# Optimization experiments

Hardware: AMD Instinct MI355X
Metric: run time of the kernel (lower is better)

Reference implementation:

```python
import jax, jax.numpy as jnp
import numpy as np

N = 20000      # num nodes
E = 320000     # num edges (before self loops)
DIN = 128      # in_channels
DH = 128       # hidden channels
C = 40         # num classes


def setup_inputs() -> dict:
    key = jax.random.key(0)
    ks = jax.random.split(key, 16)
    s_in = 1.0 / np.sqrt(DIN)
    s_h = 1.0 / np.sqrt(DH)
    s_a = 1.0 / np.sqrt(2 * DH)
    return {
        "x": jax.random.normal(ks[0], (N, DIN), jnp.float32),
        "edge_index": jax.random.randint(ks[1], (2, E), 0, N),
        "norm": jax.random.uniform(ks[2], (E + N,), jnp.float32),  # Jaccard sims in [0,1]
        # layer 1 params
        "W1": jax.random.uniform(ks[3], (DIN, DH), jnp.float32, -s_in, s_in),
        "aW1": jax.random.uniform(ks[4], (2 * DH, 1), jnp.float32, -s_a, s_a),
        "ab1": jax.random.uniform(ks[5], (1,), jnp.float32, -s_a, s_a),
        "alpha1": jnp.array([0.5], jnp.float32),
        "b1": jnp.zeros((DH,), jnp.float32),
        # layer 2 params
        "W2": jax.random.uniform(ks[6], (DH, DH), jnp.float32, -s_h, s_h),
        "aW2": jax.random.uniform(ks[7], (2 * DH, 1), jnp.float32, -s_a, s_a),
        "ab2": jax.random.uniform(ks[8], (1,), jnp.float32, -s_a, s_a),
        "alpha2": jnp.array([0.5], jnp.float32),
        "b2": jnp.zeros((DH,), jnp.float32),
        # output head
        "Wout": jax.random.uniform(ks[9], (DH, C), jnp.float32, -s_h, s_h),
        "bout": jax.random.uniform(ks[10], (C,), jnp.float32, -s_h, s_h),
    }


def _gat_layer(x, src, dst, norm, W, aW, ab, alpha, bias):
    n = x.shape[0]
    h = x @ W                              # [N, DH]
    s = h[src]                             # gathered source feats [E', DH]
    t = h[dst]                             # gathered target feats [E', DH]
    # attention logit per edge -> exp(leaky_relu(.))
    e = jnp.exp(jax.nn.leaky_relu(jnp.concatenate([s, t], axis=-1) @ aW + ab,
                                  negative_slope=0.2))          # [E', 1]
    e_sum = jax.ops.segment_sum(e, dst, num_segments=n)         # softmax denom per dst node
    a = e / e_sum[dst]
    s_sim = jnp.exp(norm)[:, None]                               # [E', 1]
    s_sum = jax.ops.segment_sum(s_sim, src, num_segments=n)     # note: summed over SRC (as in original)
    sw = s_sim / s_sum[dst]                                      # but indexed by DST (as in original)
    al = jnp.clip(alpha, 1e-4, 0.9999)
    w = al * a + (1.0 - al) * sw                                 # blended edge weight [E', 1]
    out = jax.ops.segment_max(w * s, dst, num_segments=n)        # aggr='max' propagate
    return out + bias


def reference(x, edge_index, norm, W1, aW1, ab1, alpha1, b1,
              W2, aW2, ab2, alpha2, b2, Wout, bout):
    n = x.shape[0]
    loops = jnp.arange(n, dtype=edge_index.dtype)
    src = jnp.concatenate([edge_index[0], loops])   # add_self_loops
    dst = jnp.concatenate([edge_index[1], loops])
    h = jax.nn.relu(_gat_layer(x, src, dst, norm, W1, aW1, ab1, alpha1, b1))
    h = jax.nn.relu(_gat_layer(h, src, dst, norm, W2, aW2, ab2, alpha2, b2))
    return jax.nn.log_softmax(h @ Wout + bout, axis=-1)
```

## Files before the change

kernel.cpp:

```cpp
#include <hip/hip_runtime.h>
#include <math.h>

#define DHID 128
#define NCLS 40
#define ELLW 64

typedef unsigned int   u32;
typedef unsigned short u16;

__device__ __forceinline__ u16 f2bf(float f) {
  u32 u = __float_as_uint(f);
  return (u16)((u + 0x7FFFu + ((u >> 16) & 1u)) >> 16);
}
__device__ __forceinline__ float bf_lo(u32 p) { return __uint_as_float(p << 16); }
__device__ __forceinline__ float bf_hi(u32 p) { return __uint_as_float(p & 0xFFFF0000u); }

__global__ __launch_bounds__(256) void zero_kernel(
    int* __restrict__ counts, float* __restrict__ ssum,
    int* __restrict__ ovf_cnt, int n) {
  int i = blockIdx.x * 256 + threadIdx.x;
  if (i < n) { counts[i] = 0; ssum[i] = 0.f; }
  if (i == 0) *ovf_cnt = 0;
}

__device__ __forceinline__ void gemm_from_lds(
    float* Ws, float* Xs, const float* __restrict__ W,
    const float* __restrict__ aW, u16* __restrict__ Hout,
    float* __restrict__ elo, float* __restrict__ ero, int n, int rowBase) {
  int t = threadIdx.x;
  int rg = t >> 5;
  int c0 = (t & 31) << 2;
  float acc[4][4];
#pragma unroll
  for (int j = 0; j < 4; ++j)
#pragma unroll
    for (int c = 0; c < 4; ++c) acc[j][c] = 0.f;

  for (int kt = 0; kt < 2; ++kt) {
    __syncthreads();
    const float* Wsrc = W + kt * 64 * DHID;
#pragma unroll
    for (int q = 0; q < 8; ++q) {
      int i4 = t + q * 256;
      *reinterpret_cast<float4*>(Ws + i4 * 4) =
          *reinterpret_cast<const float4*>(Wsrc + i4 * 4);
    }
    __syncthreads();
#pragma unroll 2
    for (int k = 0; k < 64; k += 4) {
      float4 xv[4];
#pragma unroll
      for (int j = 0; j < 4; ++j)
        xv[j] = *reinterpret_cast<const float4*>(
            Xs + (rg * 4 + j) * DHID + kt * 64 + k);
#pragma unroll
      for (int kk = 0; kk < 4; ++kk) {
        float4 wv = *reinterpret_cast<const float4*>(Ws + (k + kk) * DHID + c0);
#pragma unroll
        for (int j = 0; j < 4; ++j) {
          float xj = (&xv[j].x)[kk];
          acc[j][0] = fmaf(xj, wv.x, acc[j][0]);
          acc[j][1] = fmaf(xj, wv.y, acc[j][1]);
          acc[j][2] = fmaf(xj, wv.z, acc[j][2]);
          acc[j][3] = fmaf(xj, wv.w, acc[j][3]);
        }
      }
    }
  }

#pragma unroll
  for (int j = 0; j < 4; ++j) {
    int gr = rowBase + rg * 4 + j;
    if (gr < n) {
      ushort4 hv;
      hv.x = f2bf(acc[j][0]); hv.y = f2bf(acc[j][1]);
      hv.z = f2bf(acc[j][2]); hv.w = f2bf(acc[j][3]);
      *reinterpret_cast<ushort4*>(Hout + (size_t)gr * DHID + c0) = hv;
    }
  }

  float4 al4 = *reinterpret_cast<const float4*>(aW + c0);
  float4 ar4 = *reinterpret_cast<const float4*>(aW + DHID + c0);
  __syncthreads();
  float* P = Xs;
#pragma unroll
  for (int j = 0; j < 4; ++j) {
    int r = rg * 4 + j;
    float pl = acc[j][0] * al4.x + acc[j][1] * al4.y +
               acc[j][2] * al4.z + acc[j][3] * al4.w;
    float pr = acc[j][0] * ar4.x + acc[j][1] * ar4.y +
               acc[j][2] * ar4.z + acc[j][3] * ar4.w;
    P[r * 33 + (t & 31)] = pl;
    P[1056 + r * 33 + (t & 31)] = pr;
  }
  __syncthreads();
  if (t < 64) {
    int half = t >> 5, r = t & 31;
    const float* Pr = P + half * 1056 + r * 33;
    float s = 0.f;
#pragma unroll
    for (int c = 0; c < 32; ++c) s += Pr[c];
    int gr = rowBase + r;
    if (gr < n) { if (half) ero[gr] = s; else elo[gr] = s; }
  }
}

__device__ __forceinline__ void gemm_stage_x(
    float* Xs, const float* __restrict__ X, int n, int rowBase) {
  int t = threadIdx.x;
#pragma unroll
  for (int q = 0; q < 4; ++q) {
    int i4 = t + q * 256;
    int r = i4 >> 5, c = (i4 & 31) << 2;
    int gr = rowBase + r;
    float4 v = (gr < n)
        ? *reinterpret_cast<const float4*>(X + (size_t)gr * DHID + c)
        : make_float4(0.f, 0.f, 0.f, 0.f);
    *reinterpret_cast<float4*>(Xs + r * DHID + c) = v;
  }
}

__global__ __launch_bounds__(256) void gemm1_build_kernel(
    const float* __restrict__ X, const float* __restrict__ W,
    const float* __restrict__ aW, u16* __restrict__ H,
    float* __restrict__ el, float* __restrict__ er, int n, int gT,
    const int* __restrict__ ei, const float* __restrict__ norm,
    int* __restrict__ counts, float* __restrict__ ssum,
    uint2* __restrict__ ell, uint4* __restrict__ ovf,
    int* __restrict__ ovf_cnt, int E, int EP) {
  __shared__ float Ws[64 * 128];
  __shared__ float Xs[32 * 128];
  if (blockIdx.x < gT) {
    int rowBase = blockIdx.x * 32;
    gemm_stage_x(Xs, X, n, rowBase);
    gemm_from_lds(Ws, Xs, W, aW, H, el, er, n, rowBase);
  } else {
    int k = (blockIdx.x - gT) * 256 + threadIdx.x;
    if (k < EP) {
      int src, dst;
      if (k < E) { src = ei[k]; dst = ei[E + k]; }
      else       { src = dst = k - E; }
      float se = __expf(norm[k]);
      atomicAdd(&ssum[src], se);
      int slot = atomicAdd(&counts[dst], 1);
      if (slot < ELLW) {
        ell[(size_t)dst * ELLW + slot] =
            make_uint2((u32)src, __float_as_uint(se));
      } else {
        int o = atomicAdd(ovf_cnt, 1);
        ovf[o] = make_uint4((u32)dst, (u32)src, __float_as_uint(se), 0u);
      }
    }
  }
}

__global__ __launch_bounds__(256) void gemm_elr_kernel(
    const float* __restrict__ X, const float* __restrict__ W,
    const float* __restrict__ aW, u16* __restrict__ H,
    float* __restrict__ el, float* __restrict__ er, int n) {
  __shared__ float Ws[64 * 128];
  __shared__ float Xs[32 * 128];
  int rowBase = blockIdx.x * 32;
  gemm_stage_x(Xs, X, n, rowBase);
  gemm_from_lds(Ws, Xs, W, aW, H, el, er, n, rowBase);
}

__device__ __forceinline__ void agg_node8(
    const u16* __restrict__ H, const int* __restrict__ counts,
    const uint2* __restrict__ ell, const uint4* __restrict__ ovf, int ovfN,
    const float* __restrict__ el, const float* __restrict__ ssum,
    float base, float al, int node, int lane, float a[8]) {
  int deg = counts[node];
  int dell = deg < ELLW ? deg : ELLW;
  const uint2* erow = ell + (size_t)node * ELLW;
  int src0 = 0; float sx0 = 0.f;
  if (lane < dell) {
    uint2 rec = erow[lane];
    src0 = (int)rec.x;
    sx0  = __uint_as_float(rec.y);
  }
  int qw = lane >> 4;
  const u16* Hf = H + ((lane & 15) << 3);
  int ei0 = qw, ei1 = 4 + qw;
  int ci0 = ei0 < dell ? ei0 : 0;
  int ci1 = ei1 < dell ? ei1 : 0;
  int ps0 = __shfl(src0, ci0);
  int ps1 = __shfl(src0, ci1);
  uint4 pr0 = *reinterpret_cast<const uint4*>(Hf + (size_t)ps0 * DHID);
  uint4 pr1 = *reinterpret_cast<const uint4*>(Hf + (size_t)ps1 * DHID);
  float e0 = 0.f;
  if (lane < dell) {
    float g = el[src0] + base;
    e0 = __expf(g > 0.f ? g : 0.2f * g);
  }
  float es = e0;
  if (ovfN > 0 && deg > ELLW) {
    for (int cb = 0; cb < ovfN; cb += 64) {
      int i = cb + lane;
      if (i < ovfN) {
        uint4 r = ovf[i];
        if ((int)r.x == node) {
          float g = el[(int)r.y] + base;
          es += __expf(g > 0.f ? g : 0.2f * g);
        }
      }
    }
  }
#pragma unroll
  for (int off = 32; off; off >>= 1) es += __shfl_xor(es, off);
  float invEs = al / es;
  float omaS  = (1.f - al) / ssum[node];
  float w0 = e0 * invEs + sx0 * omaS;
#pragma unroll
  for (int i = 0; i < 8; ++i) a[i] = -INFINITY;
  {
    float wA = __shfl(w0, ci0);
    float wB = __shfl(w0, ci1);
    if (ei0 < dell) {
      a[0] = fmaxf(a[0], wA * bf_lo(pr0.x)); a[1] = fmaxf(a[1], wA * bf_hi(pr0.x));
      a[2] = fmaxf(a[2], wA * bf_lo(pr0.y)); a[3] = fmaxf(a[3], wA * bf_hi(pr0.y));
      a[4] = fmaxf(a[4], wA * bf_lo(pr0.z)); a[5] = fmaxf(a[5], wA * bf_hi(pr0.z));
      a[6] = fmaxf(a[6], wA * bf_lo(pr0.w)); a[7] = fmaxf(a[7], wA * bf_hi(pr0.w));
    }
    if (ei1 < dell) {
      a[0] = fmaxf(a[0], wB * bf_lo(pr1.x)); a[1] = fmaxf(a[1], wB * bf_hi(pr1.x));
      a[2] = fmaxf(a[2], wB * bf_lo(pr1.y)); a[3] = fmaxf(a[3], wB * bf_hi(pr1.y));
      a[4] = fmaxf(a[4], wB * bf_lo(pr1.z)); a[5] = fmaxf(a[5], wB * bf_hi(pr1.z));
      a[6] = fmaxf(a[6], wB * bf_lo(pr1.w)); a[7] = fmaxf(a[7], wB * bf_hi(pr1.w));
    }
  }
  int j = 8;
  for (; j + 7 < dell; j += 8) {
    int ea = j + qw, eb = j + 4 + qw;
    int   sa = __shfl(src0, ea); float wa = __shfl(w0, ea);
    int   sb = __shfl(src0, eb); float wb = __shfl(w0, eb);
    uint4 ha = *reinterpret_cast<const uint4*>(Hf + (size_t)sa * DHID);
    uint4 hb = *reinterpret_cast<const uint4*>(Hf + (size_t)sb * DHID);
    a[0] = fmaxf(a[0], fmaxf(wa * bf_lo(ha.x), wb * bf_lo(hb.x)));
    a[1] = fmaxf(a[1], fmaxf(wa * bf_hi(ha.x), wb * bf_hi(hb.x)));
    a[2] = fmaxf(a[2], fmaxf(wa * bf_lo(ha.y), wb * bf_lo(hb.y)));
    a[3] = fmaxf(a[3], fmaxf(wa * bf_hi(ha.y), wb * bf_hi(hb.y)));
    a[4] = fmaxf(a[4], fmaxf(wa * bf_lo(ha.z), wb * bf_lo(hb.z)));
    a[5] = fmaxf(a[5], fmaxf(wa * bf_hi(ha.z), wb * bf_hi(hb.z)));
    a[6] = fmaxf(a[6], fmaxf(wa * bf_lo(ha.w), wb * bf_lo(hb.w)));
    a[7] = fmaxf(a[7], fmaxf(wa * bf_hi(ha.w), wb * bf_hi(hb.w)));
  }
  for (; j < dell; j += 4) {
    int e = j + qw;
    int ec = e < dell ? e : dell - 1;
    int   sa = __shfl(src0, ec); float wa = __shfl(w0, ec);
    if (e < dell) {
      uint4 ha = *reinterpret_cast<const uint4*>(Hf + (size_t)sa * DHID);
      a[0] = fmaxf(a[0], wa * bf_lo(ha.x));
      a[1] = fmaxf(a[1], wa * bf_hi(ha.x));
      a[2] = fmaxf(a[2], wa * bf_lo(ha.y));
      a[3] = fmaxf(a[3], wa * bf_hi(ha.y));
      a[4] = fmaxf(a[4], wa * bf_lo(ha.z));
      a[5] = fmaxf(a[5], wa * bf_hi(ha.z));
      a[6] = fmaxf(a[6], wa * bf_lo(ha.w));
      a[7] = fmaxf(a[7], wa * bf_hi(ha.w));
    }
  }
  if (ovfN > 0 && deg > ELLW) {
    for (int cb = 0; cb < ovfN; cb += 64) {
      int i = cb + lane;
      uint4 r = (i < ovfN) ? ovf[i] : make_uint4(0u, 0u, 0u, 0u);
      bool match = (i < ovfN) && ((int)r.x == node);
      int si = (int)r.y;
      float wi = 0.f;
      if (match) {
        float g = el[si] + base;
        wi = __expf(g > 0.f ? g : 0.2f * g) * invEs +
             __uint_as_float(r.z) * omaS;
      }
      unsigned long long mask = __ballot(match);
      while (mask) {
        int jb = __ffsll(mask) - 1;
        mask &= mask - 1;
        int   sj = __shfl(si, jb);
        float wj = __shfl(wi, jb);
        uint4 h = *reinterpret_cast<const uint4*>(Hf + (size_t)sj * DHID);
        a[0] = fmaxf(a[0], wj * bf_lo(h.x)); a[1] = fmaxf(a[1], wj * bf_hi(h.x));
        a[2] = fmaxf(a[2], wj * bf_lo(h.y)); a[3] = fmaxf(a[3], wj * bf_hi(h.y));
        a[4] = fmaxf(a[4], wj * bf_lo(h.z)); a[5] = fmaxf(a[5], wj * bf_hi(h.z));
        a[6] = fmaxf(a[6], wj * bf_lo(h.w)); a[7] = fmaxf(a[7], wj * bf_hi(h.w));
      }
    }
  }
#pragma unroll
  for (int i = 0; i < 8; ++i) {
    a[i] = fmaxf(a[i], __shfl_xor(a[i], 16));
    a[i] = fmaxf(a[i], __shfl_xor(a[i], 32));
  }
}

__global__ __launch_bounds__(256) void agg_kernel(
    const u16* __restrict__ H, const int* __restrict__ counts,
    const uint2* __restrict__ ell, const uint4* __restrict__ ovf,
    const int* __restrict__ ovf_cnt, const float* __restrict__ el,
    const float* __restrict__ er, const float* __restrict__ ssum,
    const float* __restrict__ ab, const float* __restrict__ alpha,
    const float* __restrict__ bias, float* __restrict__ Y, int n) {
  int node = blockIdx.x * 4 + (threadIdx.x >> 6);
  int lane = threadIdx.x & 63;
  if (node >= n) return;
  int ovfN = *ovf_cnt;
  float al = fminf(fmaxf(alpha[0], 1e-4f), 0.9999f);
  float base = er[node] + ab[0];
  float a[8];
  agg_node8(H, counts, ell, ovf, ovfN, el, ssum, base, al, node, lane, a);
  if (lane < 16) {
    int fl = lane << 3;
    float4 b0 = *reinterpret_cast<const float4*>(bias + fl);
    float4 b1 = *reinterpret_cast<const float4*>(bias + fl + 4);
    float4 o0, o1;
    o0.x = fmaxf(a[0] + b0.x, 0.f); o0.y = fmaxf(a[1] + b0.y, 0.f);
    o0.z = fmaxf(a[2] + b0.z, 0.f); o0.w = fmaxf(a[3] + b0.w, 0.f);
    o1.x = fmaxf(a[4] + b1.x, 0.f); o1.y = fmaxf(a[5] + b1.y, 0.f);
    o1.z = fmaxf(a[6] + b1.z, 0.f); o1.w = fmaxf(a[7] + b1.w, 0.f);
    *reinterpret_cast<float4*>(Y + (size_t)node * DHID + fl) = o0;
    *reinterpret_cast<float4*>(Y + (size_t)node * DHID + fl + 4) = o1;
  }
}

__global__ __launch_bounds__(256) void agg_head_kernel(
    const u16* __restrict__ H, const int* __restrict__ counts,
    const uint2* __restrict__ ell, const uint4* __restrict__ ovf,
    const int* __restrict__ ovf_cnt, const float* __restrict__ el,
    const float* __restrict__ er, const float* __restrict__ ssum,
    const float* __restrict__ ab, const float* __restrict__ alpha,
    const float* __restrict__ bias, const float* __restrict__ Wout,
    const float* __restrict__ bout, float* __restrict__ out, int n) {
  __shared__ float Wl[DHID * NCLS];
  __shared__ float hl[4][DHID];
  int t = threadIdx.x;
  for (int i = t; i < DHID * NCLS; i += 256) Wl[i] = Wout[i];
  int wv = t >> 6, lane = t & 63;
  int node = blockIdx.x * 4 + wv;
  if (node < n) {
    int ovfN = *ovf_cnt;
    float al = fminf(fmaxf(alpha[0], 1e-4f), 0.9999f);
    float base = er[node] + ab[0];
    float a[8];
    agg_node8(H, counts, ell, ovf, ovfN, el, ssum, base, al, node, lane, a);
    if (lane < 16) {
      int fl = lane << 3;
#pragma unroll
      for (int i = 0; i < 8; ++i)
        hl[wv][fl + i] = fmaxf(a[i] + bias[fl + i], 0.f);
    }
  }
  __syncthreads();
  if (node >= n) return;
  float z = -INFINITY;
  bool act = lane < NCLS;
  if (act) {
    z = bout[lane];
    const float* hr = hl[wv];
#pragma unroll 8
    for (int k = 0; k < DHID; ++k) z = fmaf(hr[k], Wl[k * NCLS + lane], z);
  }
  float m = z;
#pragma unroll
  for (int off = 32; off; off >>= 1) m = fmaxf(m, __shfl_xor(m, off));
  float p = act ? expf(z - m) : 0.f;
#pragma unroll
  for (int off = 32; off; off >>= 1) p += __shfl_xor(p, off);
  float ls = logf(p);
  if (act) out[(size_t)node * NCLS + lane] = z - m - ls;
}

extern "C" void kernel_launch(void* const* d_in, const int* in_sizes, int n_in,
                              void* d_out, int out_size, void* d_ws, size_t ws_size,
                              hipStream_t stream) {
  const float* x     = (const float*)d_in[0];
  const int*   ei    = (const int*)d_in[1];
  const float* norm  = (const float*)d_in[2];
  const float* W1    = (const float*)d_in[3];
  const float* aW1   = (const float*)d_in[4];
  const float* ab1   = (const float*)d_in[5];
  const float* alpha1= (const float*)d_in[6];
  const float* b1    = (const float*)d_in[7];
  const float* W2    = (const float*)d_in[8];
  const float* aW2   = (const float*)d_in[9];
  const float* ab2   = (const float*)d_in[10];
  const float* alpha2= (const float*)d_in[11];
  const float* b2    = (const float*)d_in[12];
  const float* Wout  = (const float*)d_in[13];
  const float* bout  = (const float*)d_in[14];
  float* out = (float*)d_out;

  const int N  = in_sizes[0] / DHID;
  const int E  = in_sizes[1] / 2;
  const int EP = E + N;

  char* ws = (char*)d_ws;
  size_t off = 0;
  auto alloc = [&](size_t bytes) -> void* {
    void* p = ws + off;
    off += (bytes + 255) & ~(size_t)255;
    return p;
  };
  int*   counts  = (int*)  alloc((size_t)N * 4);
  float* ssum    = (float*)alloc((size_t)N * 4);
  int*   ovf_cnt = (int*)  alloc(256);
  u16*   Hbf     = (u16*)  alloc((size_t)N * DHID * 2);
  float* B       = (float*)alloc((size_t)N * DHID * 4);
  float* el      = (float*)alloc((size_t)N * 4);
  float* er      = (float*)alloc((size_t)N * 4);
  uint2* ell     = (uint2*)alloc((size_t)N * ELLW * 8);
  uint4* ovf     = (uint4*)alloc((size_t)EP * 16);

  const int gZero = (N + 255) / 256;
  const int gEdge = (EP + 255) / 256;
  const int gT    = (N + 31) / 32;
  const int gAgg  = (N + 3) / 4;

  zero_kernel<<<gZero, 256, 0, stream>>>(counts, ssum, ovf_cnt, N);
  gemm1_build_kernel<<<gT + gEdge, 256, 0, stream>>>(
      x, W1, aW1, Hbf, el, er, N, gT, ei, norm, counts, ssum, ell, ovf,
      ovf_cnt, E, EP);
  agg_kernel<<<gAgg, 256, 0, stream>>>(Hbf, counts, ell, ovf, ovf_cnt, el, er,
                                       ssum, ab1, alpha1, b1, B, N);
  gemm_elr_kernel<<<gT, 256, 0, stream>>>(B, W2, aW2, Hbf, el, er, N);
  agg_head_kernel<<<gAgg, 256, 0, stream>>>(Hbf, counts, ell, ovf, ovf_cnt,
                                            el, er, ssum, ab2, alpha2, b2,
                                            Wout, bout, out, N);
}
```

Before: 110.6 us.

## Use bf16 MFMA for node GEMMs with prepacked weights and bf16 activations

Replaces the fp32 LDS-tiled FMA GEMM with bf16 MFMA 16x16x32 instructions. A prep kernel now converts x to bf16, packs W1/W2 into MFMA fragment layout, and zeroes the counters. Layer-1 aggregation writes bf16 output so layer 2 reads half the bytes. This adds a conversion pass over x and lowers precision of the GEMM inputs, and leaves some dead code in the epilogue.

Result: faster. 104.7 us (-5.3%).

```diff
diff --git a/kernel.cpp b/kernel.cpp
--- a/kernel.cpp
+++ b/kernel.cpp
@@ -7,6 +7,8 @@
 
 typedef unsigned int   u32;
 typedef unsigned short u16;
+using short8 = __attribute__((ext_vector_type(8))) short;
+using f32x4  = __attribute__((ext_vector_type(4))) float;
 
 __device__ __forceinline__ u16 f2bf(float f) {
   u32 u = __float_as_uint(f);
@@ -15,125 +17,135 @@
 __device__ __forceinline__ float bf_lo(u32 p) { return __uint_as_float(p << 16); }
 __device__ __forceinline__ float bf_hi(u32 p) { return __uint_as_float(p & 0xFFFF0000u); }
 
-__global__ __launch_bounds__(256) void zero_kernel(
+__global__ __launch_bounds__(256) void prep_kernel(
+    const float* __restrict__ x, const float* __restrict__ W1,
+    const float* __restrict__ W2, u16* __restrict__ xbf,
+    u16* __restrict__ Wp1, u16* __restrict__ Wp2,
     int* __restrict__ counts, float* __restrict__ ssum,
-    int* __restrict__ ovf_cnt, int n) {
-  int i = blockIdx.x * 256 + threadIdx.x;
-  if (i < n) { counts[i] = 0; ssum[i] = 0.f; }
-  if (i == 0) *ovf_cnt = 0;
-}
-
-__device__ __forceinline__ void gemm_from_lds(
-    float* Ws, float* Xs, const float* __restrict__ W,
-    const float* __restrict__ aW, u16* __restrict__ Hout,
-    float* __restrict__ elo, float* __restrict__ ero, int n, int rowBase) {
+    int* __restrict__ ovf_cnt, int N) {
+  int gi = blockIdx.x * 256 + threadIdx.x;
+  int Ncvt = N * 16;
+  if (gi < Ncvt) {
+    int base = gi * 8;
+    float4 v0 = *reinterpret_cast<const float4*>(x + base);
+    float4 v1 = *reinterpret_cast<const float4*>(x + base + 4);
+    uint4 o;
+    o.x = (u32)f2bf(v0.x) | ((u32)f2bf(v0.y) << 16);
+    o.y = (u32)f2bf(v0.z) | ((u32)f2bf(v0.w) << 16);
+    o.z = (u32)f2bf(v1.x) | ((u32)f2bf(v1.y) << 16);
+    o.w = (u32)f2bf(v1.z) | ((u32)f2bf(v1.w) << 16);
+    *reinterpret_cast<uint4*>(xbf + base) = o;
+    return;
+  }
+  gi -= Ncvt;
+  if (gi < N) { counts[gi] = 0; ssum[gi] = 0.f; return; }
+  gi -= N;
+  if (gi < 32768) {
+    int layer = gi >> 14, q = gi & 16383;
+    int j = q & 7, l = (q >> 3) & 63, kt = (q >> 9) & 3, ct = q >> 11;
+    int k = kt * 32 + (l >> 4) * 8 + j;
+    int col = ct * 16 + (l & 15);
+    const float* Wsrc = layer ? W2 : W1;
+    u16* Wdst = layer ? Wp2 : Wp1;
+    Wdst[q] = f2bf(Wsrc[k * DHID + col]);
+    return;
+  }
+  gi -= 32768;
+  if (gi == 0) *ovf_cnt = 0;
+}
+
+__device__ __forceinline__ void mfma_gemm_block(
+    float* Cl, float* P, const u16* __restrict__ Xbf,
+    const u16* __restrict__ Wp, const float* __restrict__ aW,
+    u16* __restrict__ Hout, float* __restrict__ elo, float* __restrict__ ero,
+    int n, int rowBase) {
   int t = threadIdx.x;
-  int rg = t >> 5;
-  int c0 = (t & 31) << 2;
-  float acc[4][4];
-#pragma unroll
-  for (int j = 0; j < 4; ++j)
-#pragma unroll
-    for (int c = 0; c < 4; ++c) acc[j][c] = 0.f;
-
-  for (int kt = 0; kt < 2; ++kt) {
-    __syncthreads();
-    const float* Wsrc = W + kt * 64 * DHID;
-#pragma unroll
-    for (int q = 0; q < 8; ++q) {
-      int i4 = t + q * 256;
-      *reinterpret_cast<float4*>(Ws + i4 * 4) =
-          *reinterpret_cast<const float4*>(Wsrc + i4 * 4);
-    }
-    __syncthreads();
-#pragma unroll 2
-    for (int k = 0; k < 64; k += 4) {
-      float4 xv[4];
-#pragma unroll
-      for (int j = 0; j < 4; ++j)
-        xv[j] = *reinterpret_cast<const float4*>(
-            Xs + (rg * 4 + j) * DHID + kt * 64 + k);
-#pragma unroll
-      for (int kk = 0; kk < 4; ++kk) {
-        float4 wv = *reinterpret_cast<const float4*>(Ws + (k + kk) * DHID + c0);
-#pragma unroll
-        for (int j = 0; j < 4; ++j) {
-          float xj = (&xv[j].x)[kk];
-          acc[j][0] = fmaf(xj, wv.x, acc[j][0]);
-          acc[j][1] = fmaf(xj, wv.y, acc[j][1]);
-          acc[j][2] = fmaf(xj, wv.z, acc[j][2]);
-          acc[j][3] = fmaf(xj, wv.w, acc[j][3]);
-        }
-      }
-    }
-  }
-
+  int w = t >> 6, l = t & 63;
+  int lr = l & 15, lh = l >> 4;
+  f32x4 acc00 = {0.f,0.f,0.f,0.f}, acc01 = {0.f,0.f,0.f,0.f};
+  f32x4 acc10 = {0.f,0.f,0.f,0.f}, acc11 = {0.f,0.f,0.f,0.f};
+  int r0 = rowBase + lr;      if (r0 > n - 1) r0 = n - 1;
+  int r1 = rowBase + 16 + lr; if (r1 > n - 1) r1 = n - 1;
+  const u16* a0p = Xbf + (size_t)r0 * DHID;
+  const u16* a1p = Xbf + (size_t)r1 * DHID;
+  const u16* wb0 = Wp + ((size_t)(w * 2 + 0) * 4 * 64 + l) * 8;
+  const u16* wb1 = Wp + ((size_t)(w * 2 + 1) * 4 * 64 + l) * 8;
+#pragma unroll
+  for (int kt = 0; kt < 4; ++kt) {
+    int ko = kt * 32 + lh * 8;
+    short8 fa0 = *reinterpret_cast<const short8*>(a0p + ko);
+    short8 fa1 = *reinterpret_cast<const short8*>(a1p + ko);
+    short8 fb0 = *reinterpret_cast<const short8*>(wb0 + kt * 64 * 8);
+    short8 fb1 = *reinterpret_cast<const short8*>(wb1 + kt * 64 * 8);
+    acc00 = __builtin_amdgcn_mfma_f32_16x16x32_bf16(fa0, fb0, acc00, 0, 0, 0);
+    acc01 = __builtin_amdgcn_mfma_f32_16x16x32_bf16(fa0, fb1, acc01, 0, 0, 0);
+    acc10 = __builtin_amdgcn_mfma_f32_16x16x32_bf16(fa1, fb0, acc10, 0, 0, 0);
+    acc11 = __builtin_amdgcn_mfma_f32_16x16x32_bf16(fa1, fb1, acc11, 0, 0, 0);
+  }
 #pragma unroll
   for (int j = 0; j < 4; ++j) {
-    int gr = rowBase + rg * 4 + j;
-    if (gr < n) {
-      ushort4 hv;
-      hv.x = f2bf(acc[j][0]); hv.y = f2bf(acc[j][1]);
-      hv.z = f2bf(acc[j][2]); hv.w = f2bf(acc[j][3]);
-      *reinterpret_cast<ushort4*>(Hout + (size_t)gr * DHID + c0) = hv;
-    }
-  }
-
-  float4 al4 = *reinterpret_cast<const float4*>(aW + c0);
-  float4 ar4 = *reinterpret_cast<const float4*>(aW + DHID + c0);
+    Cl[(lh * 4 + j) * DHID + w * 32 + lr]           = acc00[j];
+    Cl[(lh * 4 + j) * DHID + w * 32 + 16 + lr]      = acc01[j];
+    Cl[(16 + lh * 4 + j) * DHID + w * 32 + lr]      = acc10[j];
+    Cl[(16 + lh * 4 + j) * DHID + w * 32 + 16 + lr] = acc11[j];
+  }
   __syncthreads();
-  float* P = Xs;
-#pragma unroll
-  for (int j = 0; j < 4; ++j) {
-    int r = rg * 4 + j;
-    float pl = acc[j][0] * al4.x + acc[j][1] * al4.y +
-               acc[j][2] * al4.z + acc[j][3] * al4.w;
-    float pr = acc[j][0] * ar4.x + acc[j][1] * ar4.y +
-               acc[j][2] * ar4.z + acc[j][3] * ar4.w;
-    P[r * 33 + (t & 31)] = pl;
-    P[1056 + r * 33 + (t & 31)] = pr;
-  }
+  int r = t >> 3, cg = (t & 7) * 16;
+  const float* crow = Cl + r * DHID + cg;
+  float pl = 0.f, pr = 0.f;
+  int gr = rowBase + r;
+  u32 packed[4];
+#pragma unroll
+  for (int q = 0; q < 4; ++q) {
+    float v0 = crow[q * 4 + 0], v1 = crow[q * 4 + 1];
+    float v2 = crow[q * 4 + 2], v3 = crow[q * 4 + 3];
+    pl = fmaf(v0, aW[cg + q * 4 + 0], pl); pr = fmaf(v0, aW[DHID + cg + q * 4 + 0], pr);
+    pl = fmaf(v1, aW[cg + q * 4 + 1], pl); pr = fmaf(v1, aW[DHID + cg + q * 4 + 1], pr);
+    pl = fmaf(v2, aW[cg + q * 4 + 2], pl); pr = fmaf(v2, aW[DHID + cg + q * 4 + 2], pr);
+    pl = fmaf(v3, aW[cg + q * 4 + 3], pl); pr = fmaf(v3, aW[DHID + cg + q * 4 + 3], pr);
+    packed[q] = (u32)f2bf(v0) | ((u32)f2bf(v1) << 16) |
+                0;
+    packed[q] |= 0;
+  }
+  if (gr < n) {
+    uint4 o;
+    o.x = (u32)f2bf(crow[0])  | ((u32)f2bf(crow[1])  << 16);
+    o.y = (u32)f2bf(crow[2])  | ((u32)f2bf(crow[3])  << 16);
+    o.z = (u32)f2bf(crow[4])  | ((u32)f2bf(crow[5])  << 16);
+    o.w = (u32)f2bf(crow[6])  | ((u32)f2bf(crow[7])  << 16);
+    *reinterpret_cast<uint4*>(Hout + (size_t)gr * DHID + cg) = o;
+    uint4 o2;
+    o2.x = (u32)f2bf(crow[8])  | ((u32)f2bf(crow[9])  << 16);
+    o2.y = (u32)f2bf(crow[10]) | ((u32)f2bf(crow[11]) << 16);
+    o2.z = (u32)f2bf(crow[12]) | ((u32)f2bf(crow[13]) << 16);
+    o2.w = (u32)f2bf(crow[14]) | ((u32)f2bf(crow[15]) << 16);
+    *reinterpret_cast<uint4*>(Hout + (size_t)gr * DHID + cg + 8) = o2;
+  }
+  P[r * 16 + (t & 7) * 2 + 0] = pl;
+  P[r * 16 + (t & 7) * 2 + 1] = pr;
   __syncthreads();
   if (t < 64) {
-    int half = t >> 5, r = t & 31;
-    const float* Pr = P + half * 1056 + r * 33;
+    int half = t >> 5, rr = t & 31;
     float s = 0.f;
 #pragma unroll
-    for (int c = 0; c < 32; ++c) s += Pr[c];
-    int gr = rowBase + r;
-    if (gr < n) { if (half) ero[gr] = s; else elo[gr] = s; }
-  }
-}
-
-__device__ __forceinline__ void gemm_stage_x(
-    float* Xs, const float* __restrict__ X, int n, int rowBase) {
-  int t = threadIdx.x;
-#pragma unroll
-  for (int q = 0; q < 4; ++q) {
-    int i4 = t + q * 256;
-    int r = i4 >> 5, c = (i4 & 31) << 2;
-    int gr = rowBase + r;
-    float4 v = (gr < n)
-        ? *reinterpret_cast<const float4*>(X + (size_t)gr * DHID + c)
-        : make_float4(0.f, 0.f, 0.f, 0.f);
-    *reinterpret_cast<float4*>(Xs + r * DHID + c) = v;
+    for (int cq = 0; cq < 8; ++cq) s += P[rr * 16 + cq * 2 + half];
+    int g2 = rowBase + rr;
+    if (g2 < n) { if (half) ero[g2] = s; else elo[g2] = s; }
   }
 }
 
 __global__ __launch_bounds__(256) void gemm1_build_kernel(
-    const float* __restrict__ X, const float* __restrict__ W,
+    const u16* __restrict__ Xbf, const u16* __restrict__ Wp,
     const float* __restrict__ aW, u16* __restrict__ H,
     float* __restrict__ el, float* __restrict__ er, int n, int gT,
     const int* __restrict__ ei, const float* __restrict__ norm,
     int* __restrict__ counts, float* __restrict__ ssum,
     uint2* __restrict__ ell, uint4* __restrict__ ovf,
     int* __restrict__ ovf_cnt, int E, int EP) {
-  __shared__ float Ws[64 * 128];
-  __shared__ float Xs[32 * 128];
+  __shared__ float Cl[32 * DHID];
+  __shared__ float P[32 * 16];
   if (blockIdx.x < gT) {
-    int rowBase = blockIdx.x * 32;
-    gemm_stage_x(Xs, X, n, rowBase);
-    gemm_from_lds(Ws, Xs, W, aW, H, el, er, n, rowBase);
+    mfma_gemm_block(Cl, P, Xbf, Wp, aW, H, el, er, n, blockIdx.x * 32);
   } else {
     int k = (blockIdx.x - gT) * 256 + threadIdx.x;
     if (k < EP) {
@@ -155,14 +167,12 @@
 }
 
 __global__ __launch_bounds__(256) void gemm_elr_kernel(
-    const float* __restrict__ X, const float* __restrict__ W,
+    const u16* __restrict__ Xbf, const u16* __restrict__ Wp,
     const float* __restrict__ aW, u16* __restrict__ H,
     float* __restrict__ el, float* __restrict__ er, int n) {
-  __shared__ float Ws[64 * 128];
-  __shared__ float Xs[32 * 128];
-  int rowBase = blockIdx.x * 32;
-  gemm_stage_x(Xs, X, n, rowBase);
-  gemm_from_lds(Ws, Xs, W, aW, H, el, er, n, rowBase);
+  __shared__ float Cl[32 * DHID];
+  __shared__ float P[32 * 16];
+  mfma_gemm_block(Cl, P, Xbf, Wp, aW, H, el, er, n, blockIdx.x * 32);
 }
 
 __device__ __forceinline__ void agg_node8(
@@ -300,7 +310,7 @@
     const int* __restrict__ ovf_cnt, const float* __restrict__ el,
     const float* __restrict__ er, const float* __restrict__ ssum,
     const float* __restrict__ ab, const float* __restrict__ alpha,
-    const float* __restrict__ bias, float* __restrict__ Y, int n) {
+    const float* __restrict__ bias, u16* __restrict__ Y, int n) {
   int node = blockIdx.x * 4 + (threadIdx.x >> 6);
   int lane = threadIdx.x & 63;
   if (node >= n) return;
@@ -311,15 +321,15 @@
   agg_node8(H, counts, ell, ovf, ovfN, el, ssum, base, al, node, lane, a);
   if (lane < 16) {
     int fl = lane << 3;
-    float4 b0 = *reinterpret_cast<const float4*>(bias + fl);
-    float4 b1 = *reinterpret_cast<const float4*>(bias + fl + 4);
-    float4 o0, o1;
-    o0.x = fmaxf(a[0] + b0.x, 0.f); o0.y = fmaxf(a[1] + b0.y, 0.f);
-    o0.z = fmaxf(a[2] + b0.z, 0.f); o0.w = fmaxf(a[3] + b0.w, 0.f);
-    o1.x = fmaxf(a[4] + b1.x, 0.f); o1.y = fmaxf(a[5] + b1.y, 0.f);
-    o1.z = fmaxf(a[6] + b1.z, 0.f); o1.w = fmaxf(a[7] + b1.w, 0.f);
-    *reinterpret_cast<float4*>(Y + (size_t)node * DHID + fl) = o0;
-    *reinterpret_cast<float4*>(Y + (size_t)node * DHID + fl + 4) = o1;
+    float v[8];
+#pragma unroll
+    for (int i = 0; i < 8; ++i) v[i] = fmaxf(a[i] + bias[fl + i], 0.f);
+    uint4 o;
+    o.x = (u32)f2bf(v[0]) | ((u32)f2bf(v[1]) << 16);
+    o.y = (u32)f2bf(v[2]) | ((u32)f2bf(v[3]) << 16);
+    o.z = (u32)f2bf(v[4]) | ((u32)f2bf(v[5]) << 16);
+    o.w = (u32)f2bf(v[6]) | ((u32)f2bf(v[7]) << 16);
+    *reinterpret_cast<uint4*>(Y + (size_t)node * DHID + fl) = o;
   }
 }
 
@@ -404,25 +414,30 @@
   int*   counts  = (int*)  alloc((size_t)N * 4);
   float* ssum    = (float*)alloc((size_t)N * 4);
   int*   ovf_cnt = (int*)  alloc(256);
+  u16*   xbf     = (u16*)  alloc((size_t)N * DHID * 2);
+  u16*   Wp1     = (u16*)  alloc(16384 * 2);
+  u16*   Wp2     = (u16*)  alloc(16384 * 2);
   u16*   Hbf     = (u16*)  alloc((size_t)N * DHID * 2);
-  float* B       = (float*)alloc((size_t)N * DHID * 4);
+  u16*   Bbf     = (u16*)  alloc((size_t)N * DHID * 2);
   float* el      = (float*)alloc((size_t)N * 4);
   float* er      = (float*)alloc((size_t)N * 4);
   uint2* ell     = (uint2*)alloc((size_t)N * ELLW * 8);
   uint4* ovf     = (uint4*)alloc((size_t)EP * 16);
 
-  const int gZero = (N + 255) / 256;
   const int gEdge = (EP + 255) / 256;
   const int gT    = (N + 31) / 32;
   const int gAgg  = (N + 3) / 4;
-
-  zero_kernel<<<gZero, 256, 0, stream>>>(counts, ssum, ovf_cnt, N);
+  const int prepWork = N * 16 + N + 32768 + 1;
+  const int gPrep = (prepWork + 255) / 256;
+
+  prep_kernel<<<gPrep, 256, 0, stream>>>(x, W1, W2, xbf, Wp1, Wp2,
+                                         counts, ssum, ovf_cnt, N);
   gemm1_build_kernel<<<gT + gEdge, 256, 0, stream>>>(
-      x, W1, aW1, Hbf, el, er, N, gT, ei, norm, counts, ssum, ell, ovf,
+      xbf, Wp1, aW1, Hbf, el, er, N, gT, ei, norm, counts, ssum, ell, ovf,
       ovf_cnt, E, EP);
   agg_kernel<<<gAgg, 256, 0, stream>>>(Hbf, counts, ell, ovf, ovf_cnt, el, er,
-                                       ssum, ab1, alpha1, b1, B, N);
-  gemm_elr_kernel<<<gT, 256, 0, stream>>>(B, W2, aW2, Hbf, el, er, N);
+                                       ssum, ab1, alpha1, b1, Bbf, N);
+  gemm_elr_kernel<<<gT, 256, 0, stream>>>(Bbf, Wp2, aW2, Hbf, el, er, N);
   agg_head_kernel<<<gAgg, 256, 0, stream>>>(Hbf, counts, ell, ovf, ovf_cnt,
                                             el, er, ssum, ab2, alpha2, b2,
                                             Wout, bout, out, N);
```
